# Kernel optimization log

Hardware: AMD Instinct MI355X
Metric: run time of the kernel (lower is better)

## Reference

```python
import jax, jax.numpy as jnp
import numpy as np

# ---- module hyperparameters (from init_kwargs / tracker defaults) ----
D_MODEL = 512
D_HEAD = 512
LAMBDA_0 = 1.0        # A_0 = I / lambda_0
FIXED_LAMBDA = 1.0    # fixed penalty magnitude -> U = sqrt(lambda) * K (then / sqrt(d_head))
STAB_EPS = 1e-6       # InversePenaltyTracker.stabilization_eps
PERIODIC_EPS = 1e-6   # InversePenaltyTracker.periodic_eps
PERIOD = 128          # InversePenaltyTracker.period (periodic re-regularization)
EXPLODE_EPS = 1e-5    # fallback_add_explode coefficient
NORM_THRESH = 1000.0  # explosion detection threshold on Frobenius norms


def setup_inputs() -> dict:
    key = jax.random.key(0)
    ks = jax.random.split(key, 9)
    B, T, d = 8, 2048, D_MODEL
    s = 1.0 / np.sqrt(d)
    f32 = jnp.float32
    return {
        "x": jax.random.normal(ks[0], (B, T, d), f32),
        "Wq": (jax.random.normal(ks[1], (D_HEAD, d), f32) * s),
        "bq": jax.random.normal(ks[2], (D_HEAD,), f32) * 0.02,
        "Wk": (jax.random.normal(ks[3], (D_HEAD, d), f32) * s),
        "bk": jax.random.normal(ks[4], (D_HEAD,), f32) * 0.02,
        "Wv": (jax.random.normal(ks[5], (D_HEAD, d), f32) * s),
        "bv": jax.random.normal(ks[6], (D_HEAD,), f32) * 0.02,
        "Wo": (jax.random.normal(ks[7], (d, D_HEAD), f32) * s),
        "bo": jax.random.normal(ks[8], (d,), f32) * 0.02,
    }


def _vla_forward(x, Wq, bq, Wk, bk, Wv, bv, Wo, bo):
    B, T, _ = x.shape
    d = D_HEAD
    # projections (nn.Linear: x @ W.T + b)
    Q = jnp.einsum('btd,hd->bth', x, Wq) + bq
    K = jnp.einsum('btd,hd->bth', x, Wk) + bk
    V = jnp.einsum('btd,hd->bth', x, Wv) + bv

    # PenaltyBuilder (rank 1, fixed lambda): u_t = sqrt(lambda) * k_t, then / sqrt(d_head)
    U = (jnp.sqrt(jnp.float32(FIXED_LAMBDA)) / jnp.sqrt(jnp.float32(d))) * K
    s_seq = jnp.sum(K * Q, axis=-1)                                   # (B,T)
    Vn = V / (jnp.linalg.norm(V, axis=-1, keepdims=True) + 1e-6)      # (B,T,d)

    I = jnp.eye(d, dtype=jnp.float32)
    A0 = jnp.zeros((B, d, d), jnp.float32) + I / LAMBDA_0
    S0 = jnp.zeros((B, d, d), jnp.float32)

    def step(carry, inp):
        A, S = carry
        q, u, s_t, vn, t = inp  # q,u,vn: (B,d); s_t: (B,); t: scalar int
        # Sherman-Morrison rank-1 inverse update with stabilization
        z = jnp.einsum('bij,bj->bi', A, u)
        dot = jnp.sum(u * z, axis=-1)
        delta = jnp.maximum(1.0 + dot, 1e-6)
        unstable = (jnp.abs(delta) < STAB_EPS) | ~jnp.isfinite(delta)
        safe = jnp.where(unstable, 1.0, delta)
        upd = (z[:, :, None] * z[:, None, :]) / safe[:, None, None]
        A = jnp.where(unstable[:, None, None], A + STAB_EPS * I, A - upd)
        # periodic re-regularization (inv_step = t+1)
        A = jnp.where(((t + 1) % PERIOD) == 0, A + PERIODIC_EPS * I, A)
        # alpha_t = s_t * (A u_t)
        z2 = jnp.einsum('bij,bj->bi', A, u)
        alpha = s_t[:, None] * z2
        # memory update S += v_norm alpha^T
        S = S + vn[:, :, None] * alpha[:, None, :]
        # explosion guard
        Sn = jnp.linalg.norm(S.reshape(S.shape[0], -1), axis=-1)
        An = jnp.linalg.norm(A.reshape(A.shape[0], -1), axis=-1)
        A = jnp.where(((Sn > NORM_THRESH) | (An > NORM_THRESH))[:, None, None],
                      A + EXPLODE_EPS * I, A)
        o = jnp.einsum('bij,bj->bi', S, q)
        return (A, S), o

    xs = (jnp.swapaxes(Q, 0, 1), jnp.swapaxes(U, 0, 1),
          jnp.swapaxes(s_seq, 0, 1), jnp.swapaxes(Vn, 0, 1),
          jnp.arange(T))
    _, O = jax.lax.scan(step, (A0, S0), xs)    # O: (T,B,d)
    O = jnp.swapaxes(O, 0, 1)                  # (B,T,d)
    return jnp.einsum('bth,dh->btd', O, Wo) + bo


def reference(x, Wq, bq, Wk, bk, Wv, bv, Wo, bo):
    return _vla_forward(x, Wq, bq, Wk, bk, Wv, bv, Wo, bo)
```

## Files before the change

### kernel.cpp

```cpp
#include <hip/hip_runtime.h>
#include <hip/hip_bf16.h>

#define BB 8
#define TT 2048
#define DD 512
#define LL 128
#define NC 16
#define ETH 512

typedef unsigned short u16;
typedef unsigned int u32;
typedef __attribute__((ext_vector_type(8))) short bf16x8v;
typedef __attribute__((ext_vector_type(4))) float f32x4v;

__device__ __forceinline__ float bf2f(u32 h) { return __uint_as_float(h << 16); }
__device__ __forceinline__ u16 f2bf(float f) {
    u32 u = __float_as_uint(f);
    u += 0x7fffu + ((u >> 16) & 1u);
    return (u16)(u >> 16);
}
__device__ __forceinline__ float wred64(float v) {
    #pragma unroll
    for (int off = 32; off; off >>= 1) v += __shfl_xor(v, off);
    return v;
}
__device__ __forceinline__ void unpack8(uint4 r, float* f) {
    f[0] = bf2f(r.x & 0xffff); f[1] = bf2f(r.x >> 16);
    f[2] = bf2f(r.y & 0xffff); f[3] = bf2f(r.y >> 16);
    f[4] = bf2f(r.z & 0xffff); f[5] = bf2f(r.z >> 16);
    f[6] = bf2f(r.w & 0xffff); f[7] = bf2f(r.w >> 16);
}

__global__ __launch_bounds__(256)
void f2bf_kernel(const float4* __restrict__ in, ushort4* __restrict__ out, const int n4)
{
    int i = blockIdx.x * 256 + threadIdx.x;
    const int stride = gridDim.x * 256;
    for (; i < n4; i += stride) {
        const float4 v = in[i];
        ushort4 o;
        o.x = f2bf(v.x); o.y = f2bf(v.y); o.z = f2bf(v.z); o.w = f2bf(v.w);
        out[i] = o;
    }
}

__global__ __launch_bounds__(256)
void wconv_kernel(const float4* __restrict__ Wq, const float4* __restrict__ Wk,
                  const float4* __restrict__ Wv, const float4* __restrict__ Wo,
                  ushort4* __restrict__ oq, ushort4* __restrict__ ok,
                  ushort4* __restrict__ ov, ushort4* __restrict__ oo)
{
    const int i = blockIdx.x * 256 + threadIdx.x;
    const int y = blockIdx.y;
    const float4* src = (y == 0) ? Wq : (y == 1) ? Wk : (y == 2) ? Wv : Wo;
    ushort4* dst = (y == 0) ? oq : (y == 1) ? ok : (y == 2) ? ov : oo;
    const float4 v = src[i];
    ushort4 o;
    o.x = f2bf(v.x); o.y = f2bf(v.y); o.z = f2bf(v.z); o.w = f2bf(v.w);
    dst[i] = o;
}

template<int OUT_BF>
__global__ __launch_bounds__(256)
void mfma_gemm(const u16* __restrict__ Abf, const u16* __restrict__ Bbf,
               const float* __restrict__ bias, void* __restrict__ Cout,
               const float outscale)
{
    __shared__ u16 Asm[128 * 64];
    __shared__ u16 Bsm[128 * 64];
    const int tid = threadIdx.x;
    const int wave = tid >> 6, lane = tid & 63;
    const int wm = wave >> 1, wn = wave & 1;
    const int m0 = blockIdx.x * 128, n0 = blockIdx.y * 128;

    f32x4v acc[4][4];
    #pragma unroll
    for (int i = 0; i < 4; ++i)
        #pragma unroll
        for (int j = 0; j < 4; ++j)
            acc[i][j] = (f32x4v){0.f, 0.f, 0.f, 0.f};

    const u16* gsrcA[4];
    const u16* gsrcB[4];
    #pragma unroll
    for (int i = 0; i < 4; ++i) {
        const int idx = i * 256 + tid;
        const int row = idx >> 3, c = idx & 7;
        const int kb = c ^ (row & 7);
        gsrcA[i] = Abf + (size_t)(m0 + row) * 512 + kb * 8;
        gsrcB[i] = Bbf + (size_t)(n0 + row) * 512 + kb * 8;
    }

    for (int k0 = 0; k0 < 512; k0 += 64) {
        __syncthreads();
        #pragma unroll
        for (int i = 0; i < 4; ++i) {
            __builtin_amdgcn_global_load_lds(
                (__attribute__((address_space(1))) void*)(gsrcA[i] + k0),
                (__attribute__((address_space(3))) void*)(Asm + (size_t)(i * 256 + wave * 64) * 8),
                16, 0, 0);
            __builtin_amdgcn_global_load_lds(
                (__attribute__((address_space(1))) void*)(gsrcB[i] + k0),
                (__attribute__((address_space(3))) void*)(Bsm + (size_t)(i * 256 + wave * 64) * 8),
                16, 0, 0);
        }
        asm volatile("s_waitcnt vmcnt(0)" ::: "memory");
        __syncthreads();

        const int l15 = lane & 15, lhi = lane >> 4;
        bf16x8v af[4][2], bfr[4][2];
        #pragma unroll
        for (int mf = 0; mf < 4; ++mf) {
            const int row = wm * 64 + mf * 16 + l15;
            const int sw = (row & 7) << 4;
            #pragma unroll
            for (int ks = 0; ks < 2; ++ks) {
                const int kbyte = ks * 64 + lhi * 16;
                af[mf][ks] = *(const bf16x8v*)((const char*)Asm + row * 128 + (kbyte ^ sw));
            }
        }
        #pragma unroll
        for (int nf = 0; nf < 4; ++nf) {
            const int row = wn * 64 + nf * 16 + l15;
            const int sw = (row & 7) << 4;
            #pragma unroll
            for (int ks = 0; ks < 2; ++ks) {
                const int kbyte = ks * 64 + lhi * 16;
                bfr[nf][ks] = *(const bf16x8v*)((const char*)Bsm + row * 128 + (kbyte ^ sw));
            }
        }
        #pragma unroll
        for (int ks = 0; ks < 2; ++ks)
            #pragma unroll
            for (int mf = 0; mf < 4; ++mf)
                #pragma unroll
                for (int nf = 0; nf < 4; ++nf)
                    acc[mf][nf] = __builtin_amdgcn_mfma_f32_16x16x32_bf16(
                        af[mf][ks], bfr[nf][ks], acc[mf][nf], 0, 0, 0);
    }
    const int l15 = lane & 15, lhi = lane >> 4;
    #pragma unroll
    for (int mf = 0; mf < 4; ++mf) {
        #pragma unroll
        for (int nf = 0; nf < 4; ++nf) {
            const int n = n0 + wn * 64 + nf * 16 + l15;
            const float bsv = bias[n];
            #pragma unroll
            for (int r = 0; r < 4; ++r) {
                const int m = m0 + wm * 64 + mf * 16 + lhi * 4 + r;
                const float val = (acc[mf][nf][r] + bsv) * outscale;
                if (OUT_BF) ((u16*)Cout)[(size_t)m * 512 + n] = f2bf(val);
                else        ((float*)Cout)[(size_t)m * 512 + n] = val;
            }
        }
    }
}

__device__ __forceinline__ void mfk6_body(const u16* __restrict__ Sb,
    const u16* __restrict__ Qt, const u16* __restrict__ AlT,
    const u16* __restrict__ Vnt, float* __restrict__ OBSA,
    float* __restrict__ dsum, const int bz)
{
    __shared__ u16 Ah[128 * 64];
    __shared__ u16 Bh[128 * 64];
    const int tid = threadIdx.x, wave = tid >> 6, lane = tid & 63;
    const int wm = wave >> 1, wn = wave & 1;
    const int m0 = blockIdx.x * 128, n0 = blockIdx.y * 128;

    f32x4v acc[4][4];
    #pragma unroll
    for (int i = 0; i < 4; ++i)
        #pragma unroll
        for (int j = 0; j < 4; ++j)
            acc[i][j] = (f32x4v){0.f, 0.f, 0.f, 0.f};

    const u16* Abase = Sb + (size_t)bz * 262144;
    const u16* Bbase = (n0 == 0) ? (Qt + (size_t)bz * 1048576)
                                 : (AlT + (size_t)bz * 65536);
    const u16* gA[4]; const u16* gB[4];
    #pragma unroll
    for (int i = 0; i < 4; ++i) {
        const int idx = i * 256 + tid, row = idx >> 3, c = idx & 7;
        const int kb = c ^ (row & 7);
        gA[i] = Abase + (size_t)(m0 + row) * 512 + kb * 8;
        gB[i] = Bbase + (size_t)row * 512 + kb * 8;
    }
    for (int k0 = 0; k0 < 512; k0 += 64) {
        __syncthreads();
        #pragma unroll
        for (int i = 0; i < 4; ++i) {
            const int dst = (i * 256 + wave * 64) * 8;
            __builtin_amdgcn_global_load_lds(
                (__attribute__((address_space(1))) void*)(gA[i] + k0),
                (__attribute__((address_space(3))) void*)(Ah + dst), 16, 0, 0);
            __builtin_amdgcn_global_load_lds(
                (__attribute__((address_space(1))) void*)(gB[i] + k0),
                (__attribute__((address_space(3))) void*)(Bh + dst), 16, 0, 0);
        }
        asm volatile("s_waitcnt vmcnt(0)" ::: "memory");
        __syncthreads();

        const int l15 = lane & 15, lhi = lane >> 4;
        bf16x8v af[4][2], bfr[4][2];
        #pragma unroll
        for (int mf = 0; mf < 4; ++mf) {
            const int row = wm * 64 + mf * 16 + l15, sw = (row & 7) << 4;
            #pragma unroll
            for (int ks = 0; ks < 2; ++ks) {
                const int kb2 = (ks * 64 + lhi * 16) ^ sw;
                af[mf][ks] = *(const bf16x8v*)((const char*)Ah + row * 128 + kb2);
            }
        }
        #pragma unroll
        for (int nf = 0; nf < 4; ++nf) {
            const int row = wn * 64 + nf * 16 + l15, sw = (row & 7) << 4;
            #pragma unroll
            for (int ks = 0; ks < 2; ++ks) {
                const int kb2 = (ks * 64 + lhi * 16) ^ sw;
                bfr[nf][ks] = *(const bf16x8v*)((const char*)Bh + row * 128 + kb2);
            }
        }
        #pragma unroll
        for (int ks = 0; ks < 2; ++ks)
            #pragma unroll
            for (int mf = 0; mf < 4; ++mf)
                #pragma unroll
                for (int nf = 0; nf < 4; ++nf)
                    acc[mf][nf] = __builtin_amdgcn_mfma_f32_16x16x32_bf16(
                        af[mf][ks], bfr[nf][ks], acc[mf][nf], 0, 0, 0);
    }
    const int l15 = lane & 15, lhi = lane >> 4;
    float* C = OBSA + (size_t)bz * 131072;
    #pragma unroll
    for (int mf = 0; mf < 4; ++mf)
        #pragma unroll
        for (int nf = 0; nf < 4; ++nf) {
            const int n = n0 + wn * 64 + nf * 16 + l15;
            #pragma unroll
            for (int r = 0; r < 4; ++r) {
                const int m = m0 + wm * 64 + mf * 16 + lhi * 4 + r;
                C[(size_t)m * 256 + n] = acc[mf][nf][r];
            }
        }
    if (n0 == 128) {
        const u16* Vn = Vnt + (size_t)bz * 1048576;
        #pragma unroll
        for (int nf = 0; nf < 4; ++nf) {
            const int n = n0 + wn * 64 + nf * 16 + l15;
            const int i2 = n - 128;
            float part = 0.f;
            #pragma unroll
            for (int mf = 0; mf < 4; ++mf) {
                const int m = m0 + wm * 64 + mf * 16 + lhi * 4;
                const ushort4 vr = *(const ushort4*)(Vn + (size_t)i2 * 512 + m);
                part += bf2f(vr.x) * acc[mf][nf][0] + bf2f(vr.y) * acc[mf][nf][1]
                      + bf2f(vr.z) * acc[mf][nf][2] + bf2f(vr.w) * acc[mf][nf][3];
            }
            part += __shfl_xor(part, 16);
            part += __shfl_xor(part, 32);
            if (lhi == 0) atomicAdd(dsum + bz * 128 + i2, part);
        }
    }
}

__global__ __launch_bounds__(256)
void prep_kernel(const u16* __restrict__ Qb, const u16* __restrict__ Ub,
                 u16* __restrict__ Vb, float* __restrict__ sseq)
{
    const int lane = threadIdx.x & 63, wid = threadIdx.x >> 6;
    const int row = blockIdx.x * 4 + wid;
    const size_t base = (size_t)row * DD;
    const uint4 qr = *(const uint4*)(Qb + base + lane * 8);
    const uint4 ur = *(const uint4*)(Ub + base + lane * 8);
    const uint4 vr = *(const uint4*)(Vb + base + lane * 8);
    float q[8], u[8], v[8];
    unpack8(qr, q); unpack8(ur, u); unpack8(vr, v);
    float sd = 0.f, nv = 0.f;
    #pragma unroll
    for (int e = 0; e < 8; ++e) { sd = fmaf(q[e], u[e], sd); nv = fmaf(v[e], v[e], nv); }
    #pragma unroll
    for (int off = 32; off; off >>= 1) { sd += __shfl_xor(sd, off); nv += __shfl_xor(nv, off); }
    if (lane == 0) sseq[row] = sd * 22.627416997969522f;
    const float inv = 1.f / (sqrtf(nv) + 1e-6f);
    uint4 o;
    o.x = (u32)f2bf(v[0] * inv) | ((u32)f2bf(v[1] * inv) << 16);
    o.y = (u32)f2bf(v[2] * inv) | ((u32)f2bf(v[3] * inv) << 16);
    o.z = (u32)f2bf(v[4] * inv) | ((u32)f2bf(v[5] * inv) << 16);
    o.w = (u32)f2bf(v[6] * inv) | ((u32)f2bf(v[7] * inv) << 16);
    *(uint4*)(Vb + base + lane * 8) = o;
}

__global__ __launch_bounds__(256)
void init_kernel(float4* __restrict__ A4, float4* __restrict__ S4,
                 ushort4* __restrict__ Sbf4,
                 float* __restrict__ SnSq, float* __restrict__ AnAcc)
{
    const int gtid = blockIdx.x * 256 + threadIdx.x;
    const int N4 = BB * DD * DD / 4;
    const ushort4 z4 = {0, 0, 0, 0};
    for (int idx = gtid; idx < N4; idx += gridDim.x * 256) {
        const int e0 = idx << 2;
        const int r = (e0 >> 9) & 511;
        const int c = e0 & 511;
        float4 v;
        v.x = (c + 0 == r) ? 1.f : 0.f;
        v.y = (c + 1 == r) ? 1.f : 0.f;
        v.z = (c + 2 == r) ? 1.f : 0.f;
        v.w = (c + 3 == r) ? 1.f : 0.f;
        A4[idx] = v;
        S4[idx] = make_float4(0.f, 0.f, 0.f, 0.f);
        Sbf4[idx] = z4;
    }
    if (gtid < BB) { SnSq[gtid] = 0.f; AnAcc[gtid] = 512.f; }
}

struct GP {
    int alay, blay, epi;
    const void* Ap; const void* Bp;
    void* Cp; float* Cio;
    const float* gdiag; float* anacc;
    const float* invdp; const float* cap; const float* cbp;
    const u16* Ulastp; float* Zsp; float* Alphap;
    u16* albt; u16* sbf;
    int lda, ldb, ldc, K;
    long sA, sB, sC, sCio;
};

__device__ __forceinline__ void gemm_body(const GP& p, const int bz) {
    __shared__ __align__(16) float As[32][68];
    __shared__ __align__(16) float Bs[32][68];
    const int m0 = blockIdx.x * 64, n0 = blockIdx.y * 64;
    const int tid = threadIdx.x, tx = tid & 15, ty = tid >> 4;
    float acc[4][4] = {};
    for (int k0 = 0; k0 < p.K; k0 += 32) {
        if (p.alay == 0) {
            const float* A = (const float*)p.Ap + (size_t)bz * p.sA;
            #pragma unroll
            for (int h = 0; h < 2; ++h) {
                const int g = tid + h * 256, m = g >> 3, k4 = (g & 7) * 4;
                const float4 r = *(const float4*)(A + (size_t)(m0 + m) * p.lda + k0 + k4);
                As[k4][m] = r.x; As[k4+1][m] = r.y; As[k4+2][m] = r.z; As[k4+3][m] = r.w;
            }
        } else if (p.alay == 2) {
            const u16* A = (const u16*)p.Ap + (size_t)bz * p.sA;
            #pragma unroll
            for (int h = 0; h < 2; ++h) {
                const int g = tid + h * 256, m = g >> 3, k4 = (g & 7) * 4;
                const ushort4 r = *(const ushort4*)(A + (size_t)(m0 + m) * p.lda + k0 + k4);
                As[k4][m]=bf2f(r.x); As[k4+1][m]=bf2f(r.y); As[k4+2][m]=bf2f(r.z); As[k4+3][m]=bf2f(r.w);
            }
        } else if (p.alay == 1 || p.alay == 4) {
            const float* A = (const float*)p.Ap + (size_t)bz * p.sA;
            #pragma unroll
            for (int h = 0; h < 2; ++h) {
                const int g = tid + h * 256, k = g >> 4, m4 = (g & 15) * 4;
                float4 r = *(const float4*)(A + (size_t)(k0 + k) * p.lda + m0 + m4);
                if (p.alay == 4) {
                    const int kg = k0 + k, mg = m0 + m4;
                    if (kg > mg + 0) r.x = 0.f;
                    if (kg > mg + 1) r.y = 0.f;
                    if (kg > mg + 2) r.z = 0.f;
                    if (kg > mg + 3) r.w = 0.f;
                }
                As[k][m4] = r.x; As[k][m4+1] = r.y; As[k][m4+2] = r.z; As[k][m4+3] = r.w;
            }
        } else {
            const u16* A = (const u16*)p.Ap + (size_t)bz * p.sA;
            #pragma unroll
            for (int h = 0; h < 2; ++h) {
                const int g = tid + h * 256, k = g >> 4, m4 = (g & 15) * 4;
                const ushort4 r = *(const ushort4*)(A + (size_t)(k0 + k) * p.lda + m0 + m4);
                As[k][m4]=bf2f(r.x); As[k][m4+1]=bf2f(r.y); As[k][m4+2]=bf2f(r.z); As[k][m4+3]=bf2f(r.w);
            }
        }
        if (p.blay == 0) {
            const float* B = (const float*)p.Bp + (size_t)bz * p.sB;
            #pragma unroll
            for (int h = 0; h < 2; ++h) {
                const int g = tid + h * 256, k = g >> 4, n4 = (g & 15) * 4;
                const float4 r = *(const float4*)(B + (size_t)(k0 + k) * p.ldb + n0 + n4);
                Bs[k][n4] = r.x; Bs[k][n4+1] = r.y; Bs[k][n4+2] = r.z; Bs[k][n4+3] = r.w;
            }
        } else if (p.blay == 2) {
            const u16* B = (const u16*)p.Bp + (size_t)bz * p.sB;
            #pragma unroll
            for (int h = 0; h < 2; ++h) {
                const int g = tid + h * 256, k = g >> 4, n4 = (g & 15) * 4;
                const ushort4 r = *(const ushort4*)(B + (size_t)(k0 + k) * p.ldb + n0 + n4);
                Bs[k][n4]=bf2f(r.x); Bs[k][n4+1]=bf2f(r.y); Bs[k][n4+2]=bf2f(r.z); Bs[k][n4+3]=bf2f(r.w);
            }
        } else if (p.blay == 1) {
            const float* B = (const float*)p.Bp + (size_t)bz * p.sB;
            #pragma unroll
            for (int h = 0; h < 2; ++h) {
                const int g = tid + h * 256, n = g >> 3, k4 = (g & 7) * 4;
                const float4 r = *(const float4*)(B + (size_t)(n0 + n) * p.ldb + k0 + k4);
                Bs[k4][n] = r.x; Bs[k4+1][n] = r.y; Bs[k4+2][n] = r.z; Bs[k4+3][n] = r.w;
            }
        } else {
            const u16* B = (const u16*)p.Bp + (size_t)bz * p.sB;
            #pragma unroll
            for (int h = 0; h < 2; ++h) {
                const int g = tid + h * 256, n = g >> 3, k4 = (g & 7) * 4;
                const ushort4 r = *(const ushort4*)(B + (size_t)(n0 + n) * p.ldb + k0 + k4);
                Bs[k4][n]=bf2f(r.x); Bs[k4+1][n]=bf2f(r.y); Bs[k4+2][n]=bf2f(r.z); Bs[k4+3][n]=bf2f(r.w);
            }
        }
        __syncthreads();
        #pragma unroll
        for (int kk = 0; kk < 32; ++kk) {
            const float4 xa = *(const float4*)&As[kk][ty * 4];
            const float4 wb = *(const float4*)&Bs[kk][tx * 4];
            const float xv[4] = {xa.x, xa.y, xa.z, xa.w};
            const float wv[4] = {wb.x, wb.y, wb.z, wb.w};
            #pragma unroll
            for (int i = 0; i < 4; ++i)
                #pragma unroll
                for (int j = 0; j < 4; ++j)
                    acc[i][j] = fmaf(xv[i], wv[j], acc[i][j]);
        }
        __syncthreads();
    }
    const int mb = m0 + ty * 4, nb = n0 + tx * 4;
    if (p.epi == 0) {
        float* C = (float*)p.Cp + (size_t)bz * p.sC;
        #pragma unroll
        for (int i = 0; i < 4; ++i)
            #pragma unroll
            for (int j = 0; j < 4; ++j)
                C[(size_t)(mb + i) * p.ldc + nb + j] = acc[i][j];
    } else if (p.epi == 1) {
        float* C = p.Cio + (size_t)bz * p.sCio;
        const float gd = p.gdiag[bz];
        float v2 = 0.f;
        #pragma unroll
        for (int i = 0; i < 4; ++i)
            #pragma unroll
            for (int j = 0; j < 4; ++j) {
                const size_t idx = (size_t)(mb + i) * p.ldc + nb + j;
                float v = C[idx] - acc[i][j] + ((mb + i) == (nb + j) ? gd : 0.f);
                C[idx] = v;
                v2 = fmaf(v, v, v2);
            }
        v2 = wred64(v2);
        if ((tid & 63) == 0) atomicAdd(p.anacc + bz, v2);
    } else if (p.epi == 2) {
        float* C = p.Cio + (size_t)bz * p.sCio;
        u16* SB = p.sbf + (size_t)bz * p.sCio;
        #pragma unroll
        for (int i = 0; i < 4; ++i)
            #pragma unroll
            for (int j = 0; j < 4; ++j) {
                const size_t idx = (size_t)(mb + i) * p.ldc + nb + j;
                const float v = C[idx] + acc[i][j];
                C[idx] = v;
                SB[idx] = f2bf(v);
            }
    } else if (p.epi == 3) {
        u16* O = (u16*)p.Cp + (size_t)bz * p.sC;
        const float* OB = p.Cio + (size_t)bz * p.sCio;
        #pragma unroll
        for (int i = 0; i < 4; ++i)
            #pragma unroll
            for (int j = 0; j < 4; ++j)
                O[(size_t)(mb + i) * p.ldc + nb + j] =
                    f2bf(acc[i][j] + OB[(size_t)(nb + j) * 256 + mb + i]);
    } else {
        float* Zb  = (float*)p.Cp + (size_t)bz * 65536;
        float* Zsb = p.Zsp + (size_t)bz * 65536;
        float* Apb = p.Alphap + (size_t)bz * 65536;
        #pragma unroll
        for (int j = 0; j < 4; ++j) {
            const int n = nb + j;
            const float iv = p.invdp[bz * 128 + n];
            const float cav = p.cap[bz * 128 + n];
            const float cbv = p.cbp[bz * 128 + n];
            #pragma unroll
            for (int i = 0; i < 4; ++i) {
                const int m = mb + i;
                const float z = acc[i][j];
                const size_t o = (size_t)m * 128 + n;
                Zb[o] = z;
                Zsb[o] = z * iv;
                float a = z * cav;
                if (cbv != 0.f) a = fmaf(cbv, bf2f(p.Ulastp[(size_t)bz * 1048576 + m]), a);
                Apb[o] = a;
                p.albt[(size_t)bz * 65536 + (size_t)n * 512 + m] = f2bf(a);
            }
        }
    }
}

__global__ __launch_bounds__(256) void gemmx(GP p) { gemm_body(p, blockIdx.z); }

__global__ __launch_bounds__(256)
void lvl5_kernel(const u16* Sb, const u16* AlT, const float* Alpha,
                 const u16* Qt, const u16* Vnt,
                 float* P, float* Ga, float* Gv, float* OBSA, float* dsum)
{
    const int z = blockIdx.z;
    if (z < 8) {
        mfk6_body(Sb, Qt, AlT, Vnt, OBSA, dsum, z);
        return;
    }
    if (blockIdx.x >= 2 || blockIdx.y >= 2) return;
    const int zz = z - 8, b = zz / 3, j = zz - b * 3;
    GP p{};
    p.K = 512; p.epi = 0; p.ldc = 128; p.sC = 16384;
    if (j == 0) {
        p.alay = 1; p.Ap = Alpha; p.lda = 128; p.sA = 65536;
        p.blay = 3; p.Bp = Qt; p.ldb = 512; p.sB = 1048576; p.Cp = P;
    } else if (j == 1) {
        p.alay = 1; p.Ap = Alpha; p.lda = 128; p.sA = 65536;
        p.blay = 0; p.Bp = Alpha; p.ldb = 128; p.sB = 65536; p.Cp = Ga;
    } else {
        p.alay = 2; p.Ap = Vnt; p.lda = 512; p.sA = 1048576;
        p.blay = 3; p.Bp = Vnt; p.ldb = 512; p.sB = 1048576; p.Cp = Gv;
    }
    gemm_body(p, b);
}

__global__ __launch_bounds__(256)
void lvl7_kernel(const float* P, const u16* Vnt, u16* Obt, const float* OBSA,
                 const float* Alpha, const float* Zs, const float* Z,
                 float* S, u16* Sbf, float* A, const float* gdiag, float* AnAcc)
{
    const int z = blockIdx.z;
    GP p{};
    if (z < 8) {
        p.alay = 0; p.Ap = Zs; p.lda = 128; p.sA = 65536;
        p.blay = 1; p.Bp = Z; p.ldb = 128; p.sB = 65536;
        p.epi = 1; p.Cio = A; p.sCio = 262144; p.ldc = 512;
        p.gdiag = gdiag; p.anacc = AnAcc; p.K = 128;
        gemm_body(p, z);
    } else if (z < 16) {
        p.alay = 3; p.Ap = Vnt; p.lda = 512; p.sA = 1048576;
        p.blay = 1; p.Bp = Alpha; p.ldb = 128; p.sB = 65536;
        p.epi = 2; p.Cio = S; p.sbf = Sbf; p.sCio = 262144; p.ldc = 512; p.K = 128;
        gemm_body(p, z - 8);
    } else {
        if (blockIdx.x >= 2) return;
        p.alay = 4; p.Ap = P; p.lda = 128; p.sA = 16384;
        p.blay = 2; p.Bp = Vnt; p.ldb = 512; p.sB = 1048576;
        p.epi = 3; p.Cp = Obt; p.ldc = 512; p.sC = 1048576;
        p.Cio = (float*)OBSA; p.sCio = 131072; p.K = 128;
        gemm_body(p, z - 16);
    }
}

__global__ __launch_bounds__(512)
void elim_kernel(const float* __restrict__ G, float* __restrict__ Tg,
                 const float* __restrict__ sseq, float* __restrict__ invd,
                 float* __restrict__ ca, float* __restrict__ cb,
                 float* __restrict__ dsum_g, const int t0)
{
    const int b = blockIdx.x, tid = threadIdx.x, lane = tid & 63, wave = tid >> 6;
    __shared__ __align__(16) float E[128][132];
    __shared__ __align__(16) float Cs[128][132];
    __shared__ __align__(16) float LpT[8][132];
    __shared__ __align__(16) float SpT[8][132];
    __shared__ float Msc[8][8][9];
    __shared__ float del[128];
    float (*Tm)[132] = E;

    {
        const float4* Gb = (const float4*)(G + (size_t)b * 16384);
        for (int idx = tid; idx < 4096; idx += ETH) {
            const int r = idx >> 5, c4 = idx & 31;
            ((float4*)&E[r][0])[c4] = Gb[idx];
        }
    }
    if (tid < 128) dsum_g[b * 128 + tid] = 0.f;
    __syncthreads();

    for (int p = 0; p < 16; ++p) {
        const int pc0 = p * 8;
        if (wave == 0) {
            float pr0[8], pr1[8];
            #pragma unroll
            for (int j = 0; j < 8; ++j) {
                pr0[j] = E[pc0 + j][lane];
                pr1[j] = E[pc0 + j][64 + lane];
            }
            float dl[8];
            const bool hi = (pc0 >= 64);
            #pragma unroll
            for (int j = 0; j < 8; ++j) {
                const int t = pc0 + j;
                const int pl = t & 63;
                float prow[8];
                #pragma unroll
                for (int c = 0; c < 8; ++c) {
                    const float v0 = __shfl(pr0[c], pl);
                    const float v1 = __shfl(pr1[c], pl);
                    prow[c] = hi ? v1 : v0;
                }
                const float d = fmaxf(1.f + prow[j], 1e-6f);
                dl[j] = d;
                const float inv = 1.f / d;
                if (lane > t) {
                    const float coef = pr0[j] * inv;
                    #pragma unroll
                    for (int c = j + 1; c < 8; ++c) pr0[c] = fmaf(-coef, prow[c], pr0[c]);
                }
                if (lane + 64 > t) {
                    const float coef = pr1[j] * inv;
                    #pragma unroll
                    for (int c = j + 1; c < 8; ++c) pr1[c] = fmaf(-coef, prow[c], pr1[c]);
                }
            }
            #pragma unroll
            for (int j = 0; j < 8; ++j) {
                const float idj = 1.f / dl[j];
                const int t = pc0 + j;
                {
                    const bool below = (lane > t);
                    const float y = below ? pr0[j] : 0.f;
                    const float l = y * idj;
                    LpT[j][lane] = l; SpT[j][lane] = y; Cs[t][lane] = l;
                }
                {
                    const int r = lane + 64;
                    const bool below = (r > t);
                    const float y = below ? pr1[j] : 0.f;
                    const float l = y * idj;
                    LpT[j][r] = l; SpT[j][r] = y; Cs[t][r] = l;
                }
            }
            if (lane < 8) del[pc0 + lane] = dl[lane];
        }
        __syncthreads();
        const int r0b = pc0 + 8;
        if (r0b < 128) {
            const int nrows = 128 - r0b;
            const int c40 = r0b >> 2, nc4 = 32 - c40;
            for (int idx = tid; idx < nrows * nc4; idx += ETH) {
                const int rr = idx / nc4, cc = idx - rr * nc4;
                const int r = r0b + rr, c4 = c40 + cc;
                float4 e = ((float4*)&E[r][0])[c4];
                #pragma unroll
                for (int j = 0; j < 8; ++j) {
                    const float lv = LpT[j][r];
                    const float4 sv = ((const float4*)&SpT[j][0])[c4];
                    e.x = fmaf(-lv, sv.x, e.x);
                    e.y = fmaf(-lv, sv.y, e.y);
                    e.z = fmaf(-lv, sv.z, e.z);
                    e.w = fmaf(-lv, sv.w, e.w);
                }
                ((float4*)&E[r][0])[c4] = e;
            }
        }
        __syncthreads();
    }

    for (int idx = tid; idx < 4224; idx += ETH)
        ((float4*)&Tm[0][0])[idx] = make_float4(0.f, 0.f, 0.f, 0.f);
    __syncthreads();
    if (tid < 128) Tm[tid][tid] = 1.f;
    __syncthreads();
    {
        const int g = tid >> 3, c = tid & 7;
        if (g < 16) {
            for (int r2 = c - 1; r2 >= 0; --r2) {
                float s = 0.f;
                for (int kk = r2 + 1; kk <= c; ++kk)
                    s = fmaf(Cs[8 * g + r2][8 * g + kk],
                             (kk == c) ? 1.f : Tm[8 * g + kk][8 * g + c], s);
                Tm[8 * g + r2][8 * g + c] = -s;
            }
        }
    }
    __syncthreads();
    const int rr8 = lane >> 3, cc8 = lane & 7;
    #pragma unroll
    for (int which = 0; which < 2; ++which) {
        const int j = which ? (15 - wave) : wave;
        for (int i = j - 1; i >= 0; --i) {
            float m = 0.f;
            for (int l = i + 1; l <= j; ++l) {
                #pragma unroll
                for (int kk = 0; kk < 8; ++kk)
                    m = fmaf(Cs[8 * i + rr8][8 * l + kk], Tm[8 * l + kk][8 * j + cc8], m);
            }
            Msc[wave][rr8][cc8] = m;
            float s = 0.f;
            #pragma unroll
            for (int kk = 0; kk < 8; ++kk)
                s = fmaf(Tm[8 * i + rr8][8 * i + kk], Msc[wave][kk][cc8], s);
            Tm[8 * i + rr8][8 * j + cc8] = -s;
        }
    }
    __syncthreads();
    {
        float4* Tgb = (float4*)(Tg + (size_t)b * 16384);
        for (int idx = tid; idx < 4096; idx += ETH) {
            const int r = idx >> 5, c4 = idx & 31;
            Tgb[idx] = ((const float4*)&Tm[r][0])[c4];
        }
    }
    if (tid < 128) {
        const float d = del[tid];
        const float s = sseq[(size_t)b * TT + t0 + tid];
        invd[b * 128 + tid] = 1.f / d;
        ca[b * 128 + tid] = s / d;
        cb[b * 128 + tid] = (tid == 127) ? s * 1e-6f : 0.f;
    }
}

__global__ __launch_bounds__(256)
void guard_kernel(const float* __restrict__ dsum_g, const float* __restrict__ Ga,
                  const float* __restrict__ Gv, float* __restrict__ SnSq,
                  float* __restrict__ AnAcc, float* __restrict__ gdiag)
{
    const int b = blockIdx.x, tid = threadIdx.x;
    __shared__ float rpart[256], dsh[128], mdia[128];
    const int t = tid & 127, half = tid >> 7;
    const float* gv = Gv + (size_t)b * 16384 + t * 128;
    const float* ga = Ga + (size_t)b * 16384 + t * 128;
    float rs = 0.f;
    for (int j = half; j < t; j += 2) rs = fmaf(gv[j], ga[j], rs);
    rpart[tid] = rs;
    if (half == 0) { dsh[t] = dsum_g[b * 128 + t]; mdia[t] = gv[t] * ga[t]; }
    __syncthreads();
    if (tid == 0) {
        const float An2 = AnAcc[b];
        float Sn2 = SnSq[b], D = 0.f, T = 0.f;
        int ng = 0;
        for (int t2 = 0; t2 < 128; ++t2) {
            D += dsh[t2];
            T += mdia[t2] + 2.f * (rpart[t2] + rpart[t2 + 128]);
            const float sn2 = Sn2 + 2.f * D + T;
            if (sn2 > 1e6f || An2 > 1e6f) ++ng;
        }
        SnSq[b] = Sn2 + 2.f * D + T;
        gdiag[b] = 1e-6f + (float)ng * 1e-5f;
        AnAcc[b] = 0.f;
    }
}

extern "C" void kernel_launch(void* const* d_in, const int* in_sizes, int n_in,
                              void* d_out, int out_size, void* d_ws, size_t ws_size,
                              hipStream_t stream)
{
    const float* x  = (const float*)d_in[0];
    const float* Wq = (const float*)d_in[1];
    const float* bq = (const float*)d_in[2];
    const float* Wk = (const float*)d_in[3];
    const float* bk = (const float*)d_in[4];
    const float* Wv = (const float*)d_in[5];
    const float* bv = (const float*)d_in[6];
    const float* Wo = (const float*)d_in[7];
    const float* bo = (const float*)d_in[8];

    char* ws = (char*)d_ws;
    u16* Qb    = (u16*)(ws);
    u16* Ub    = (u16*)(ws + (16ull << 20));
    u16* Vnb   = (u16*)(ws + (32ull << 20));
    u16* Ob    = (u16*)(ws + (48ull << 20));
    u16* x_bf  = Ob;
    float* A    = (float*)(ws + (64ull << 20));
    float* S    = (float*)(ws + (72ull << 20));
    float* Wm   = (float*)(ws + (80ull << 20));
    float* Z    = (float*)(ws + (82ull << 20));
    float* Zs   = (float*)(ws + (84ull << 20));
    float* Alpha= (float*)(ws + (86ull << 20));
    float* OBSA = (float*)(ws + (88ull << 20));
    float* G    = (float*)(ws + (92ull << 20));
    float* Tg   = (float*)(ws + (92ull << 20) + (512ull << 10));
    float* P    = (float*)(ws + (93ull << 20));
    float* Ga   = (float*)(ws + (93ull << 20) + (512ull << 10));
    float* Gv   = (float*)(ws + (94ull << 20));
    float* invd = (float*)(ws + (94ull << 20) + (512ull << 10));
    float* ca   = (float*)(ws + (94ull << 20) + (516ull << 10));
    float* cb   = (float*)(ws + (94ull << 20) + (520ull << 10));
    float* sseq = (float*)(ws + (94ull << 20) + (528ull << 10));
    float* SnSq = (float*)(ws + (94ull << 20) + (600ull << 10));
    float* AnAcc= (float*)(ws + (94ull << 20) + (600ull << 10) + 64);
    float* gdiag= (float*)(ws + (94ull << 20) + (600ull << 10) + 128);
    float* dsum = (float*)(ws + (94ull << 20) + (604ull << 10));
    u16* Wq_bf = (u16*)(ws + (95ull << 20));
    u16* Wk_bf = (u16*)(ws + (95ull << 20) + (512ull << 10));
    u16* Wv_bf = (u16*)(ws + (96ull << 20));
    u16* Wo_bf = (u16*)(ws + (96ull << 20) + (512ull << 10));
    u16* S_bf  = (u16*)(ws + (97ull << 20));
    u16* AlT   = (u16*)(ws + (101ull << 20));

    f2bf_kernel<<<2048, 256, 0, stream>>>((const float4*)x, (ushort4*)x_bf, 2097152);
    wconv_kernel<<<dim3(256, 4), 256, 0, stream>>>(
        (const float4*)Wq, (const float4*)Wk, (const float4*)Wv, (const float4*)Wo,
        (ushort4*)Wq_bf, (ushort4*)Wk_bf, (ushort4*)Wv_bf, (ushort4*)Wo_bf);

    mfma_gemm<1><<<dim3(128, 4), 256, 0, stream>>>(x_bf, Wq_bf, bq, Qb, 1.f);
    mfma_gemm<1><<<dim3(128, 4), 256, 0, stream>>>(x_bf, Wk_bf, bk, Ub, 0.04419417382415922f);
    mfma_gemm<1><<<dim3(128, 4), 256, 0, stream>>>(x_bf, Wv_bf, bv, Vnb, 1.f);
    prep_kernel<<<4096, 256, 0, stream>>>(Qb, Ub, Vnb, sseq);
    init_kernel<<<2048, 256, 0, stream>>>((float4*)A, (float4*)S, (ushort4*)S_bf, SnSq, AnAcc);

    for (int c = 0; c < NC; ++c) {
        const int t0 = c * LL;
        const u16* Ut = Ub + (size_t)t0 * 512;
        const u16* Qt = Qb + (size_t)t0 * 512;
        const u16* Vt = Vnb + (size_t)t0 * 512;
        GP p1{}; p1.alay = 0; p1.Ap = A; p1.lda = 512; p1.sA = 262144;
        p1.blay = 3; p1.Bp = Ut; p1.ldb = 512; p1.sB = 1048576;
        p1.epi = 0; p1.Cp = Wm; p1.ldc = 128; p1.sC = 65536; p1.K = 512;
        gemmx<<<dim3(8, 2, 8), 256, 0, stream>>>(p1);
        GP p2{}; p2.alay = 2; p2.Ap = Ut; p2.lda = 512; p2.sA = 1048576;
        p2.blay = 0; p2.Bp = Wm; p2.ldb = 128; p2.sB = 65536;
        p2.epi = 0; p2.Cp = G; p2.ldc = 128; p2.sC = 16384; p2.K = 512;
        gemmx<<<dim3(2, 2, 8), 256, 0, stream>>>(p2);
        elim_kernel<<<8, 512, 0, stream>>>(G, Tg, sseq, invd, ca, cb, dsum, t0);
        GP p4{}; p4.alay = 0; p4.Ap = Wm; p4.lda = 128; p4.sA = 65536;
        p4.blay = 0; p4.Bp = Tg; p4.ldb = 128; p4.sB = 16384;
        p4.epi = 4; p4.Cp = Z; p4.Zsp = Zs; p4.Alphap = Alpha; p4.albt = AlT;
        p4.invdp = invd; p4.cap = ca; p4.cbp = cb;
        p4.Ulastp = Ub + (size_t)(t0 + 127) * 512;
        p4.K = 128; p4.ldc = 128; p4.sC = 65536;
        gemmx<<<dim3(8, 2, 8), 256, 0, stream>>>(p4);
        lvl5_kernel<<<dim3(4, 2, 32), 256, 0, stream>>>(S_bf, AlT, Alpha, Qt, Vt,
            P, Ga, Gv, OBSA, dsum);
        guard_kernel<<<8, 256, 0, stream>>>(dsum, Ga, Gv, SnSq, AnAcc, gdiag);
        lvl7_kernel<<<dim3(8, 8, 24), 256, 0, stream>>>(P, Vt, Ob + (size_t)t0 * 512, OBSA,
            Alpha, Zs, Z, S, S_bf, A, gdiag, AnAcc);
    }
    mfma_gemm<0><<<dim3(128, 4), 256, 0, stream>>>(Ob, Wo_bf, bo, d_out, 1.f);
}
```

Before: 3.662 ms.

## Use bf16 MFMA for A·U product and blocked doubling for triangular inverse

Keeps a bf16 copy of the inverse matrix A, written in the A-update epilogue and initialized in init_kernel. When the workspace is large enough, the per-chunk A·U^T product then runs on a new MFMA kernel with swizzled LDS tiles loaded via global_load_lds, replacing the fp32 scalar gemm. Separately, the triangular-inverse step in elim_kernel switches from a per-wave sequential block back-substitution to a recursive doubling scheme with more parallel work per stage. The bf16 A lowers precision of a recurrent quantity, and the new path only runs if ws_size is at least 111 MB.

```diff
diff --git a/kernel.cpp b/kernel.cpp
--- a/kernel.cpp
+++ b/kernel.cpp
@@ -264,6 +264,93 @@
 }
 
 __global__ __launch_bounds__(256)
+void mfk1_kernel(const u16* __restrict__ Abf, const u16* __restrict__ Ut,
+                 float* __restrict__ Wm)
+{
+    __shared__ u16 Ah[128 * 64];
+    __shared__ u16 Bh[128 * 64];
+    const int tid = threadIdx.x, wave = tid >> 6, lane = tid & 63;
+    const int wm = wave >> 1, wn = wave & 1;
+    const int m0 = blockIdx.x * 128;
+    const int bz = blockIdx.z;
+
+    f32x4v acc[4][4];
+    #pragma unroll
+    for (int i = 0; i < 4; ++i)
+        #pragma unroll
+        for (int j = 0; j < 4; ++j)
+            acc[i][j] = (f32x4v){0.f, 0.f, 0.f, 0.f};
+
+    const u16* Abase = Abf + (size_t)bz * 262144;
+    const u16* Bbase = Ut + (size_t)bz * 1048576;
+    const u16* gA[4]; const u16* gB[4];
+    #pragma unroll
+    for (int i = 0; i < 4; ++i) {
+        const int idx = i * 256 + tid, row = idx >> 3, c = idx & 7;
+        const int kb = c ^ (row & 7);
+        gA[i] = Abase + (size_t)(m0 + row) * 512 + kb * 8;
+        gB[i] = Bbase + (size_t)row * 512 + kb * 8;
+    }
+    for (int k0 = 0; k0 < 512; k0 += 64) {
+        __syncthreads();
+        #pragma unroll
+        for (int i = 0; i < 4; ++i) {
+            const int dst = (i * 256 + wave * 64) * 8;
+            __builtin_amdgcn_global_load_lds(
+                (__attribute__((address_space(1))) void*)(gA[i] + k0),
+                (__attribute__((address_space(3))) void*)(Ah + dst), 16, 0, 0);
+            __builtin_amdgcn_global_load_lds(
+                (__attribute__((address_space(1))) void*)(gB[i] + k0),
+                (__attribute__((address_space(3))) void*)(Bh + dst), 16, 0, 0);
+        }
+        asm volatile("s_waitcnt vmcnt(0)" ::: "memory");
+        __syncthreads();
+
+        const int l15 = lane & 15, lhi = lane >> 4;
+        bf16x8v af[4][2], bfr[4][2];
+        #pragma unroll
+        for (int mf = 0; mf < 4; ++mf) {
+            const int row = wm * 64 + mf * 16 + l15, sw = (row & 7) << 4;
+            #pragma unroll
+            for (int ks = 0; ks < 2; ++ks) {
+                const int kb2 = (ks * 64 + lhi * 16) ^ sw;
+                af[mf][ks] = *(const bf16x8v*)((const char*)Ah + row * 128 + kb2);
+            }
+        }
+        #pragma unroll
+        for (int nf = 0; nf < 4; ++nf) {
+            const int row = wn * 64 + nf * 16 + l15, sw = (row & 7) << 4;
+            #pragma unroll
+            for (int ks = 0; ks < 2; ++ks) {
+                const int kb2 = (ks * 64 + lhi * 16) ^ sw;
+                bfr[nf][ks] = *(const bf16x8v*)((const char*)Bh + row * 128 + kb2);
+            }
+        }
+        #pragma unroll
+        for (int ks = 0; ks < 2; ++ks)
+            #pragma unroll
+            for (int mf = 0; mf < 4; ++mf)
+                #pragma unroll
+                for (int nf = 0; nf < 4; ++nf)
+                    acc[mf][nf] = __builtin_amdgcn_mfma_f32_16x16x32_bf16(
+                        af[mf][ks], bfr[nf][ks], acc[mf][nf], 0, 0, 0);
+    }
+    const int l15 = lane & 15, lhi = lane >> 4;
+    float* C = Wm + (size_t)bz * 65536;
+    #pragma unroll
+    for (int mf = 0; mf < 4; ++mf)
+        #pragma unroll
+        for (int nf = 0; nf < 4; ++nf) {
+            const int n = wn * 64 + nf * 16 + l15;
+            #pragma unroll
+            for (int r = 0; r < 4; ++r) {
+                const int m = m0 + wm * 64 + mf * 16 + lhi * 4 + r;
+                C[(size_t)m * 128 + n] = acc[mf][nf][r];
+            }
+        }
+}
+
+__global__ __launch_bounds__(256)
 void prep_kernel(const u16* __restrict__ Qb, const u16* __restrict__ Ub,
                  u16* __restrict__ Vb, float* __restrict__ sseq)
 {
@@ -292,7 +379,7 @@
 
 __global__ __launch_bounds__(256)
 void init_kernel(float4* __restrict__ A4, float4* __restrict__ S4,
-                 ushort4* __restrict__ Sbf4,
+                 ushort4* __restrict__ Sbf4, ushort4* __restrict__ Abf4,
                  float* __restrict__ SnSq, float* __restrict__ AnAcc)
 {
     const int gtid = blockIdx.x * 256 + threadIdx.x;
@@ -310,6 +397,14 @@
         A4[idx] = v;
         S4[idx] = make_float4(0.f, 0.f, 0.f, 0.f);
         Sbf4[idx] = z4;
+        if (Abf4) {
+            ushort4 a;
+            a.x = (c + 0 == r) ? 0x3F80 : 0;
+            a.y = (c + 1 == r) ? 0x3F80 : 0;
+            a.z = (c + 2 == r) ? 0x3F80 : 0;
+            a.w = (c + 3 == r) ? 0x3F80 : 0;
+            Abf4[idx] = a;
+        }
     }
     if (gtid < BB) { SnSq[gtid] = 0.f; AnAcc[gtid] = 512.f; }
 }
@@ -321,7 +416,7 @@
     const float* gdiag; float* anacc;
     const float* invdp; const float* cap; const float* cbp;
     const u16* Ulastp; float* Zsp; float* Alphap;
-    u16* albt; u16* sbf;
+    u16* albt; u16* sbf; u16* abf;
     int lda, ldb, ldc, K;
     long sA, sB, sC, sCio;
 };
@@ -440,6 +535,7 @@
                 const size_t idx = (size_t)(mb + i) * p.ldc + nb + j;
                 float v = C[idx] - acc[i][j] + ((mb + i) == (nb + j) ? gd : 0.f);
                 C[idx] = v;
+                if (p.abf) p.abf[(size_t)bz * p.sCio + idx] = f2bf(v);
                 v2 = fmaf(v, v, v2);
             }
         v2 = wred64(v2);
@@ -523,7 +619,8 @@
 __global__ __launch_bounds__(256)
 void lvl7_kernel(const float* P, const u16* Vnt, u16* Obt, const float* OBSA,
                  const float* Alpha, const float* Zs, const float* Z,
-                 float* S, u16* Sbf, float* A, const float* gdiag, float* AnAcc)
+                 float* S, u16* Sbf, float* A, u16* Abf,
+                 const float* gdiag, float* AnAcc)
 {
     const int z = blockIdx.z;
     GP p{};
@@ -531,7 +628,7 @@
         p.alay = 0; p.Ap = Zs; p.lda = 128; p.sA = 65536;
         p.blay = 1; p.Bp = Z; p.ldb = 128; p.sB = 65536;
         p.epi = 1; p.Cio = A; p.sCio = 262144; p.ldc = 512;
-        p.gdiag = gdiag; p.anacc = AnAcc; p.K = 128;
+        p.gdiag = gdiag; p.anacc = AnAcc; p.abf = Abf; p.K = 128;
         gemm_body(p, z);
     } else if (z < 16) {
         p.alay = 3; p.Ap = Vnt; p.lda = 512; p.sA = 1048576;
@@ -557,11 +654,11 @@
     const int b = blockIdx.x, tid = threadIdx.x, lane = tid & 63, wave = tid >> 6;
     __shared__ __align__(16) float E[128][132];
     __shared__ __align__(16) float Cs[128][132];
-    __shared__ __align__(16) float LpT[8][132];
-    __shared__ __align__(16) float SpT[8][132];
-    __shared__ float Msc[8][8][9];
+    __shared__ __align__(16) float Scr[2368];
     __shared__ float del[128];
     float (*Tm)[132] = E;
+    float (*LpT)[132] = (float(*)[132])Scr;
+    float (*SpT)[132] = (float(*)[132])(Scr + 1056);
 
     {
         const float4* Gb = (const float4*)(G + (size_t)b * 16384);
@@ -671,26 +768,52 @@
         }
     }
     __syncthreads();
-    const int rr8 = lane >> 3, cc8 = lane & 7;
-    #pragma unroll
-    for (int which = 0; which < 2; ++which) {
-        const int j = which ? (15 - wave) : wave;
-        for (int i = j - 1; i >= 0; --i) {
-            float m = 0.f;
-            for (int l = i + 1; l <= j; ++l) {
-                #pragma unroll
-                for (int kk = 0; kk < 8; ++kk)
-                    m = fmaf(Cs[8 * i + rr8][8 * l + kk], Tm[8 * l + kk][8 * j + cc8], m);
-            }
-            Msc[wave][rr8][cc8] = m;
-            float s = 0.f;
-            #pragma unroll
-            for (int kk = 0; kk < 8; ++kk)
-                s = fmaf(Tm[8 * i + rr8][8 * i + kk], Msc[wave][kk][cc8], s);
-            Tm[8 * i + rr8][8 * j + cc8] = -s;
-        }
-    }
-    __syncthreads();
+    for (int s = 8; s <= 64; s <<= 1) {
+        const int npairs = 64 / s;
+        const int nj = (s == 64) ? 32 : s;
+        const int stride = nj + 4;
+        const int nj4 = nj >> 2;
+        const int Nel = npairs * s * nj4;
+        const int nhalf = (s == 64) ? 2 : 1;
+        for (int jh = 0; jh < nhalf; ++jh) {
+            for (int idx = tid; idx < Nel; idx += ETH) {
+                const int p2 = idx / (s * nj4), rem = idx - p2 * s * nj4;
+                const int i = rem / nj4, j4 = rem - i * nj4;
+                const int I0 = 2 * s * p2, J0 = I0 + s;
+                const int jc = j4 * 4 + jh * 32;
+                float4 x = make_float4(0.f, 0.f, 0.f, 0.f);
+                for (int k = 0; k < s; ++k) {
+                    const float cv = Cs[I0 + i][J0 + k];
+                    const float4 tv = *(const float4*)&Tm[J0 + k][J0 + jc];
+                    x.x = fmaf(cv, tv.x, x.x);
+                    x.y = fmaf(cv, tv.y, x.y);
+                    x.z = fmaf(cv, tv.z, x.z);
+                    x.w = fmaf(cv, tv.w, x.w);
+                }
+                *(float4*)&Scr[p2 * s * stride + i * stride + j4 * 4] = x;
+            }
+            __syncthreads();
+            for (int idx = tid; idx < Nel; idx += ETH) {
+                const int p2 = idx / (s * nj4), rem = idx - p2 * s * nj4;
+                const int i = rem / nj4, j4 = rem - i * nj4;
+                const int I0 = 2 * s * p2, J0 = I0 + s;
+                const int jc = j4 * 4 + jh * 32;
+                float4 y = make_float4(0.f, 0.f, 0.f, 0.f);
+                for (int k = 0; k < s; ++k) {
+                    const float tv = Tm[I0 + i][I0 + k];
+                    const float4 xv = *(const float4*)&Scr[p2 * s * stride + k * stride + j4 * 4];
+                    y.x = fmaf(tv, xv.x, y.x);
+                    y.y = fmaf(tv, xv.y, y.y);
+                    y.z = fmaf(tv, xv.z, y.z);
+                    y.w = fmaf(tv, xv.w, y.w);
+                }
+                float4 o;
+                o.x = -y.x; o.y = -y.y; o.z = -y.z; o.w = -y.w;
+                *(float4*)&Tm[I0 + i][J0 + jc] = o;
+            }
+            __syncthreads();
+        }
+    }
     {
         float4* Tgb = (float4*)(Tg + (size_t)b * 16384);
         for (int idx = tid; idx < 4096; idx += ETH) {
@@ -785,6 +908,9 @@
     u16* S_bf  = (u16*)(ws + (97ull << 20));
     u16* AlT   = (u16*)(ws + (101ull << 20));
 
+    const bool big = (ws_size >= (111ull << 20));
+    u16* A_bf = big ? (u16*)(ws + (102ull << 20)) : (u16*)nullptr;
+
     f2bf_kernel<<<2048, 256, 0, stream>>>((const float4*)x, (ushort4*)x_bf, 2097152);
     wconv_kernel<<<dim3(256, 4), 256, 0, stream>>>(
         (const float4*)Wq, (const float4*)Wk, (const float4*)Wv, (const float4*)Wo,
@@ -794,17 +920,22 @@
     mfma_gemm<1><<<dim3(128, 4), 256, 0, stream>>>(x_bf, Wk_bf, bk, Ub, 0.04419417382415922f);
     mfma_gemm<1><<<dim3(128, 4), 256, 0, stream>>>(x_bf, Wv_bf, bv, Vnb, 1.f);
     prep_kernel<<<4096, 256, 0, stream>>>(Qb, Ub, Vnb, sseq);
-    init_kernel<<<2048, 256, 0, stream>>>((float4*)A, (float4*)S, (ushort4*)S_bf, SnSq, AnAcc);
+    init_kernel<<<2048, 256, 0, stream>>>((float4*)A, (float4*)S, (ushort4*)S_bf,
+                                          (ushort4*)A_bf, SnSq, AnAcc);
 
     for (int c = 0; c < NC; ++c) {
         const int t0 = c * LL;
         const u16* Ut = Ub + (size_t)t0 * 512;
         const u16* Qt = Qb + (size_t)t0 * 512;
         const u16* Vt = Vnb + (size_t)t0 * 512;
-        GP p1{}; p1.alay = 0; p1.Ap = A; p1.lda = 512; p1.sA = 262144;
-        p1.blay = 3; p1.Bp = Ut; p1.ldb = 512; p1.sB = 1048576;
-        p1.epi = 0; p1.Cp = Wm; p1.ldc = 128; p1.sC = 65536; p1.K = 512;
-        gemmx<<<dim3(8, 2, 8), 256, 0, stream>>>(p1);
+        if (big) {
+            mfk1_kernel<<<dim3(4, 1, 8), 256, 0, stream>>>(A_bf, Ut, Wm);
+        } else {
+            GP p1{}; p1.alay = 0; p1.Ap = A; p1.lda = 512; p1.sA = 262144;
+            p1.blay = 3; p1.Bp = Ut; p1.ldb = 512; p1.sB = 1048576;
+            p1.epi = 0; p1.Cp = Wm; p1.ldc = 128; p1.sC = 65536; p1.K = 512;
+            gemmx<<<dim3(8, 2, 8), 256, 0, stream>>>(p1);
+        }
         GP p2{}; p2.alay = 2; p2.Ap = Ut; p2.lda = 512; p2.sA = 1048576;
         p2.blay = 0; p2.Bp = Wm; p2.ldb = 128; p2.sB = 65536;
         p2.epi = 0; p2.Cp = G; p2.ldc = 128; p2.sC = 16384; p2.K = 512;
@@ -821,7 +952,7 @@
             P, Ga, Gv, OBSA, dsum);
         guard_kernel<<<8, 256, 0, stream>>>(dsum, Ga, Gv, SnSq, AnAcc, gdiag);
         lvl7_kernel<<<dim3(8, 8, 24), 256, 0, stream>>>(P, Vt, Ob + (size_t)t0 * 512, OBSA,
-            Alpha, Zs, Z, S, S_bf, A, gdiag, AnAcc);
+            Alpha, Zs, Z, S, S_bf, A, A_bf, gdiag, AnAcc);
     }
     mfma_gemm<0><<<dim3(128, 4), 256, 0, stream>>>(Ob, Wo_bf, bo, d_out, 1.f);
 }
```

Result: faster. 3.366 ms (-8.1%).
